# Kernel tuning notes

Hardware: AMD Instinct MI355X
Metric: run time of the kernel (lower is better)

Reference implementation:

```python
import jax, jax.numpy as jnp
import numpy as np

LN_EPS = 1e-5


def layernorm(x, gamma, beta):
    mu = x.mean(-1, keepdims=True)
    var = x.var(-1, keepdims=True)
    return (x - mu) / jnp.sqrt(var + LN_EPS) * gamma + beta


def setup_inputs() -> dict:
    key = jax.random.key(0)
    ks = jax.random.split(key, 8)
    B, S, H, F, V = 4, 512, 1024, 512, 32000
    def sc(k, shape, fan):
        return jax.random.normal(k, shape, jnp.float32) * (1.0 / np.sqrt(fan))
    return {
        "h": jax.random.normal(ks[0], (B, S, H), jnp.float32),
        "embedding_matrix": sc(ks[1], (V, F), F),
        "output_bias": jnp.zeros((V,), jnp.float32),
        "labels": jax.random.randint(ks[2], (B, S), 0, V),
        "W_hidden": sc(ks[3], (F, H), H),
        "b_hidden": jnp.zeros((F,), jnp.float32),
        "hidden_bias": jnp.zeros((F,), jnp.float32),
        "W_proj": sc(ks[4], (F, F), F),
        "projection_bias": jnp.zeros((F,), jnp.float32),
        "ln_gamma": jnp.ones((F,), jnp.float32),
        "ln_beta": jnp.zeros((F,), jnp.float32),
        "step_W": jnp.ones((F, F), jnp.float32),
        "step_b": jnp.ones((F,), jnp.float32),
    }


def _token_nll(logits, labels):
    # per-token cross entropy, reduction='none'
    logp = jax.nn.log_softmax(logits, axis=-1)
    return -jnp.take_along_axis(logp, labels[..., None], axis=-1)[..., 0]


def reference(h, embedding_matrix, output_bias, labels, W_hidden, b_hidden,
              hidden_bias, W_proj, projection_bias, ln_gamma, ln_beta,
              step_W, step_b):
    # ---- slow path + grads of summed slow loss wrt 4 params ----
    def slow_loss(Wh, hb, Wp, bp):
        v = jax.nn.relu(h @ Wh.T + b_hidden + hb)          # [B,S,F]
        o = layernorm(v @ Wp.T + bp, ln_gamma, ln_beta)    # [B,S,F]
        logits = o @ embedding_matrix.T + output_bias      # [B,S,V]
        return _token_nll(logits, labels).sum()

    gWh, ghb, gWp, gbp = jax.grad(slow_loss, argnums=(0, 1, 2, 3))(
        W_hidden, hidden_bias, W_proj, projection_bias)

    # ---- fast-weight path, vectorized over all timesteps ----
    # Per token: fast_w = W_proj - step_W * (v v^T) @ gWp
    #   (v v^T) @ gWp = outer(v, u) with u = v @ gWp, so
    #   v @ fast_w.T = v @ W_proj.T - v * ((v*u) @ step_W.T)   (no [F,F] per token)
    v = jax.nn.relu(h @ W_hidden.T + b_hidden + hidden_bias)  # [B,S,F]
    u = jnp.einsum('bsf,fg->bsg', v, gWp)                     # v^T gWp
    o_pre = v @ W_proj.T - v * jnp.einsum('bsf,gf->bsg', v * u, step_W)
    # fast_b = projection_bias - step_b * (v v^T) @ gbp = bp - step_b * v * (v.gbp)
    fast_b = projection_bias - step_b * v * (v @ gbp)[..., None]
    o_fast = layernorm(o_pre + fast_b, ln_gamma, ln_beta)     # [B,S,F]

    logits_fast = o_fast @ embedding_matrix.T + output_bias   # [B,S,V]
    fast_loss = _token_nll(logits_fast, labels)               # [B,S]
    return (fast_loss, gWh, ghb, gWp, gbp)
```

## Files before the change

kernel.cpp:

```cpp
#include <hip/hip_runtime.h>
#include <cstddef>
#include <math.h>

#define T_TOK 2048
#define F_DIM 512
#define H_DIM 1024
#define V_DIM 32000
#define VHALF 16000
#define NKC   5
#define KC    3200
#define LN_EPS 1e-5f
#define SHIFT 20.0f

typedef __attribute__((ext_vector_type(8))) short bf16x8;
typedef __attribute__((ext_vector_type(4))) float f32x4;

__device__ __forceinline__ unsigned short f2bf(float x) {
  unsigned int u = __float_as_uint(x);
  u += 0x7fffu + ((u >> 16) & 1u);
  return (unsigned short)(u >> 16);
}

__device__ __forceinline__ void gld16(const unsigned short* gsrc, unsigned short* ldst) {
  __builtin_amdgcn_global_load_lds(
      (const __attribute__((address_space(1))) unsigned int*)gsrc,
      (__attribute__((address_space(3))) unsigned int*)ldst, 16, 0, 0);
}

__device__ inline float wave_sum(float x) {
#pragma unroll
  for (int off = 32; off > 0; off >>= 1) x += __shfl_xor(x, off, 64);
  return x;
}

__global__ void zero_kernel(float* __restrict__ p, int n) {
  int i = blockIdx.x * 256 + threadIdx.x;
  if (i < n) p[i] = 0.f;
}

__global__ void zero4_kernel(float4* __restrict__ p, int n4) {
  int i = blockIdx.x * 256 + threadIdx.x;
  if (i < n4) {
    float4 z; z.x = 0.f; z.y = 0.f; z.z = 0.f; z.w = 0.f;
    p[i] = z;
  }
}

__global__ __launch_bounds__(256) void reduceK_kernel(
    const float4* __restrict__ parts, float4* __restrict__ out, int n4, int nslab) {
  const int i = blockIdx.x * 256 + threadIdx.x;
  if (i >= n4) return;
  float4 s = parts[i];
  for (int k = 1; k < nslab; ++k) {
    float4 p = parts[(size_t)k * n4 + i];
    s.x += p.x; s.y += p.y; s.z += p.z; s.w += p.w;
  }
  out[i] = s;
}

__global__ __launch_bounds__(256) void convT_kernel(
    const float* __restrict__ in, unsigned short* __restrict__ out, int R, int C) {
  __shared__ unsigned short tile[64][65];
  const int r0 = blockIdx.x * 64, c0 = blockIdx.y * 64;
  const int rr = threadIdx.x >> 4, cc4 = (threadIdx.x & 15) * 4;
#pragma unroll
  for (int ps = 0; ps < 4; ++ps) {
    const int row = ps * 16 + rr;
    float4 x = *(const float4*)&in[(size_t)(r0 + row) * C + c0 + cc4];
    tile[row][cc4 + 0] = f2bf(x.x); tile[row][cc4 + 1] = f2bf(x.y);
    tile[row][cc4 + 2] = f2bf(x.z); tile[row][cc4 + 3] = f2bf(x.w);
  }
  __syncthreads();
#pragma unroll
  for (int ps = 0; ps < 4; ++ps) {
    const int orow = ps * 16 + rr;
    ushort4 u;
    u.x = tile[cc4 + 0][orow]; u.y = tile[cc4 + 1][orow];
    u.z = tile[cc4 + 2][orow]; u.w = tile[cc4 + 3][orow];
    *(ushort4*)&out[(size_t)(c0 + orow) * R + r0 + cc4] = u;
  }
}

__global__ __launch_bounds__(256) void convertE_kernel(
    const float* __restrict__ E, unsigned short* __restrict__ Ebf,
    unsigned short* __restrict__ Etbf)
{
  __shared__ float tile[64][65];
  const int tid = threadIdx.x;
  const int v0 = blockIdx.x * 64, f0 = blockIdx.y * 64;
  const int r = tid >> 4, cq = (tid & 15) * 4;
#pragma unroll
  for (int ps = 0; ps < 4; ++ps) {
    const int row = ps * 16 + r;
    float4 x = *(const float4*)&E[(size_t)(v0 + row) * F_DIM + f0 + cq];
    tile[row][cq + 0] = x.x; tile[row][cq + 1] = x.y;
    tile[row][cq + 2] = x.z; tile[row][cq + 3] = x.w;
    ushort4 u; u.x = f2bf(x.x); u.y = f2bf(x.y); u.z = f2bf(x.z); u.w = f2bf(x.w);
    *(ushort4*)&Ebf[(size_t)(v0 + row) * F_DIM + f0 + cq] = u;
  }
  __syncthreads();
#pragma unroll
  for (int ps = 0; ps < 4; ++ps) {
    const int frow = ps * 16 + r;
    ushort4 u;
    u.x = f2bf(tile[cq + 0][frow]); u.y = f2bf(tile[cq + 1][frow]);
    u.z = f2bf(tile[cq + 2][frow]); u.w = f2bf(tile[cq + 3][frow]);
    *(ushort4*)&Etbf[(size_t)(f0 + frow) * V_DIM + v0 + cq] = u;
  }
}

__global__ __launch_bounds__(256, 2) void gemm_bf_nt_kernel(
    const unsigned short* __restrict__ A, const unsigned short* __restrict__ B,
    int M, int N, int K,
    const float* __restrict__ maskv,
    float* __restrict__ outf, int atomic_f)
{
  __shared__ __align__(16) unsigned short As[128 * 64];
  __shared__ __align__(16) unsigned short Bs[128 * 64];
  const int tid = threadIdx.x;
  const int w = tid >> 6, lane = tid & 63;
  const int c15 = lane & 15, q = lane >> 4;
  const int n0 = blockIdx.x * 128, m0 = blockIdx.y * 128;
  const int kc = K / gridDim.z;
  const int kbase = blockIdx.z * kc;
  const int mw = (w & 1) * 64, nw = (w >> 1) * 64;
  f32x4 acc[4][4];
#pragma unroll
  for (int mi = 0; mi < 4; ++mi)
#pragma unroll
    for (int nj = 0; nj < 4; ++nj) acc[mi][nj] = (f32x4){0.f, 0.f, 0.f, 0.f};
  for (int it = 0; it < kc / 64; ++it) {
    const int kb = kbase + it * 64;
#pragma unroll
    for (int i = 0; i < 4; ++i) {
      const int gid = (w * 4 + i) * 64 + lane;
      const int row = gid >> 3, col = gid & 7;
      const int colsrc = col ^ (row & 7);
      gld16(A + (size_t)(m0 + row) * K + kb + colsrc * 8, &As[(w * 4 + i) * 512]);
      gld16(B + (size_t)(n0 + row) * K + kb + colsrc * 8, &Bs[(w * 4 + i) * 512]);
    }
    __syncthreads();
#pragma unroll
    for (int kk = 0; kk < 2; ++kk) {
      const int g = (kk * 4 + q) ^ (c15 & 7);
      bf16x8 af[4], bfr[4];
#pragma unroll
      for (int mi = 0; mi < 4; ++mi) {
        const int row = mw + mi * 16 + c15;
        af[mi] = *(const bf16x8*)&As[(row * 8 + g) * 8];
      }
#pragma unroll
      for (int nj = 0; nj < 4; ++nj) {
        const int row = nw + nj * 16 + c15;
        bfr[nj] = *(const bf16x8*)&Bs[(row * 8 + g) * 8];
      }
#pragma unroll
      for (int mi = 0; mi < 4; ++mi)
#pragma unroll
        for (int nj = 0; nj < 4; ++nj)
          acc[mi][nj] = __builtin_amdgcn_mfma_f32_16x16x32_bf16(af[mi], bfr[nj], acc[mi][nj], 0, 0, 0);
    }
    __syncthreads();
  }
#pragma unroll
  for (int mi = 0; mi < 4; ++mi)
#pragma unroll
    for (int nj = 0; nj < 4; ++nj) {
      const int n = n0 + nw + nj * 16 + c15;
#pragma unroll
      for (int r = 0; r < 4; ++r) {
        const int m = m0 + mw + mi * 16 + q * 4 + r;
        const size_t idx = (size_t)m * N + n;
        float v = acc[mi][nj][r];
        if (maskv && !(maskv[idx] > 0.f)) v = 0.f;
        if (atomic_f) atomicAdd(outf + idx, v); else outf[idx] = v;
      }
    }
}

__global__ __launch_bounds__(256) void gemm_nt_kernel(
    const float* __restrict__ A, const float* __restrict__ A2,
    const float* __restrict__ B, float* __restrict__ C,
    int M, int N, int K,
    const float* __restrict__ bias1, const float* __restrict__ bias2, int relu)
{
  __shared__ float As[16][68];
  __shared__ float Bs[16][68];
  const int tid = threadIdx.x;
  const int m0 = blockIdx.y * 64, n0 = blockIdx.x * 64;
  const int ty = tid >> 4, tx = tid & 15;
  const int lrow = tid >> 2, lkq = (tid & 3) * 4;
  float acc[4][4] = {};
  for (int k0 = 0; k0 < K; k0 += 16) {
    float4 a4 = *(const float4*)(A + (size_t)(m0 + lrow) * K + k0 + lkq);
    if (A2) {
      float4 u4 = *(const float4*)(A2 + (size_t)(m0 + lrow) * K + k0 + lkq);
      a4.x *= u4.x; a4.y *= u4.y; a4.z *= u4.z; a4.w *= u4.w;
    }
    float4 b4 = *(const float4*)(B + (size_t)(n0 + lrow) * K + k0 + lkq);
    As[lkq+0][lrow] = a4.x; As[lkq+1][lrow] = a4.y; As[lkq+2][lrow] = a4.z; As[lkq+3][lrow] = a4.w;
    Bs[lkq+0][lrow] = b4.x; Bs[lkq+1][lrow] = b4.y; Bs[lkq+2][lrow] = b4.z; Bs[lkq+3][lrow] = b4.w;
    __syncthreads();
#pragma unroll
    for (int k = 0; k < 16; ++k) {
      float4 a = *(const float4*)&As[k][ty*4];
      float4 b = *(const float4*)&Bs[k][tx*4];
      float ar[4] = {a.x,a.y,a.z,a.w}, br[4] = {b.x,b.y,b.z,b.w};
#pragma unroll
      for (int i = 0; i < 4; ++i)
#pragma unroll
        for (int j = 0; j < 4; ++j) acc[i][j] = fmaf(ar[i], br[j], acc[i][j]);
    }
    __syncthreads();
  }
#pragma unroll
  for (int i = 0; i < 4; ++i) {
    const int m = m0 + ty*4 + i;
    float cr[4];
#pragma unroll
    for (int j = 0; j < 4; ++j) {
      const int n = n0 + tx*4 + j;
      float v = acc[i][j];
      if (bias1) v += bias1[n];
      if (bias2) v += bias2[n];
      if (relu) v = fmaxf(v, 0.f);
      cr[j] = v;
    }
    float4 c; c.x = cr[0]; c.y = cr[1]; c.z = cr[2]; c.w = cr[3];
    *(float4*)(C + (size_t)m * N + n0 + tx*4) = c;
  }
}

__global__ __launch_bounds__(256) void gemm_nn_kernel(
    const float* __restrict__ A, const float* __restrict__ B,
    float* __restrict__ C, int M, int N, int K)
{
  __shared__ float As[16][68];
  __shared__ float Bs[16][68];
  const int tid = threadIdx.x;
  const int m0 = blockIdx.y * 64, n0 = blockIdx.x * 64;
  const int ty = tid >> 4, tx = tid & 15;
  const int arow = tid >> 2, akq = (tid & 3) * 4;
  const int brow = tid >> 4, bcq = (tid & 15) * 4;
  float acc[4][4] = {};
  for (int k0 = 0; k0 < K; k0 += 16) {
    float4 a4 = *(const float4*)(A + (size_t)(m0 + arow) * K + k0 + akq);
    float4 b4 = *(const float4*)(B + (size_t)(k0 + brow) * N + n0 + bcq);
    As[akq+0][arow] = a4.x; As[akq+1][arow] = a4.y; As[akq+2][arow] = a4.z; As[akq+3][arow] = a4.w;
    *(float4*)&Bs[brow][bcq] = b4;
    __syncthreads();
#pragma unroll
    for (int k = 0; k < 16; ++k) {
      float4 a = *(const float4*)&As[k][ty*4];
      float4 b = *(const float4*)&Bs[k][tx*4];
      float ar[4] = {a.x,a.y,a.z,a.w}, br[4] = {b.x,b.y,b.z,b.w};
#pragma unroll
      for (int i = 0; i < 4; ++i)
#pragma unroll
        for (int j = 0; j < 4; ++j) acc[i][j] = fmaf(ar[i], br[j], acc[i][j]);
    }
    __syncthreads();
  }
#pragma unroll
  for (int i = 0; i < 4; ++i) {
    const int m = m0 + ty*4 + i;
    float4 c; c.x = acc[i][0]; c.y = acc[i][1]; c.z = acc[i][2]; c.w = acc[i][3];
    *(float4*)(C + (size_t)m * N + n0 + tx*4) = c;
  }
}

__global__ __launch_bounds__(256) void gemm_tn_kernel(
    const float* __restrict__ A, const float* __restrict__ B,
    float* __restrict__ C, int M, int N, int K)
{
  __shared__ float As[16][68];
  __shared__ float Bs[16][68];
  const int tid = threadIdx.x;
  const int m0 = blockIdx.y * 64, n0 = blockIdx.x * 64;
  const int ty = tid >> 4, tx = tid & 15;
  const int row = tid >> 4, cq = (tid & 15) * 4;
  const int kc = K / gridDim.z;
  const int kbase = blockIdx.z * kc;
  float* __restrict__ Co = C + (size_t)blockIdx.z * M * N;
  float acc[4][4] = {};
  for (int k0 = kbase; k0 < kbase + kc; k0 += 16) {
    float4 a4 = *(const float4*)(A + (size_t)(k0 + row) * M + m0 + cq);
    float4 b4 = *(const float4*)(B + (size_t)(k0 + row) * N + n0 + cq);
    *(float4*)&As[row][cq] = a4;
    *(float4*)&Bs[row][cq] = b4;
    __syncthreads();
#pragma unroll
    for (int k = 0; k < 16; ++k) {
      float4 a = *(const float4*)&As[k][ty*4];
      float4 b = *(const float4*)&Bs[k][tx*4];
      float ar[4] = {a.x,a.y,a.z,a.w}, br[4] = {b.x,b.y,b.z,b.w};
#pragma unroll
      for (int i = 0; i < 4; ++i)
#pragma unroll
        for (int j = 0; j < 4; ++j) acc[i][j] = fmaf(ar[i], br[j], acc[i][j]);
    }
    __syncthreads();
  }
#pragma unroll
  for (int i = 0; i < 4; ++i) {
    const int m = m0 + ty*4 + i;
    float4 c; c.x = acc[i][0]; c.y = acc[i][1]; c.z = acc[i][2]; c.w = acc[i][3];
    *(float4*)(Co + (size_t)m * N + n0 + tx*4) = c;
  }
}

__global__ __launch_bounds__(256) void ln_fwd_kernel(
    const float* __restrict__ p, const float* __restrict__ v,
    const float* __restrict__ tmat, const float* __restrict__ stepb,
    const float* __restrict__ sdot, const float* __restrict__ gamma,
    const float* __restrict__ beta, float* __restrict__ o,
    unsigned short* __restrict__ obf,
    float* __restrict__ mu_out, float* __restrict__ rstd_out, int fastmode)
{
  const int t = blockIdx.x * 4 + (threadIdx.x >> 6);
  const int lane = threadIdx.x & 63;
  const int f0 = lane * 4, f1 = 256 + lane * 4;
  const float* pr = p + (size_t)t * F_DIM;
  float4 x0 = *(const float4*)(pr + f0);
  float4 x1 = *(const float4*)(pr + f1);
  if (fastmode) {
    const float* vr = v + (size_t)t * F_DIM;
    const float* tr = tmat + (size_t)t * F_DIM;
    const float sdt = sdot[t];
    float4 v0 = *(const float4*)(vr + f0), v1 = *(const float4*)(vr + f1);
    float4 t0 = *(const float4*)(tr + f0), t1 = *(const float4*)(tr + f1);
    float4 s0 = *(const float4*)(stepb + f0), s1 = *(const float4*)(stepb + f1);
    x0.x -= v0.x * (t0.x + s0.x * sdt);
    x0.y -= v0.y * (t0.y + s0.y * sdt);
    x0.z -= v0.z * (t0.z + s0.z * sdt);
    x0.w -= v0.w * (t0.w + s0.w * sdt);
    x1.x -= v1.x * (t1.x + s1.x * sdt);
    x1.y -= v1.y * (t1.y + s1.y * sdt);
    x1.z -= v1.z * (t1.z + s1.z * sdt);
    x1.w -= v1.w * (t1.w + s1.w * sdt);
  }
  float s  = x0.x + x0.y + x0.z + x0.w + x1.x + x1.y + x1.z + x1.w;
  float ss = x0.x*x0.x + x0.y*x0.y + x0.z*x0.z + x0.w*x0.w
           + x1.x*x1.x + x1.y*x1.y + x1.z*x1.z + x1.w*x1.w;
  s = wave_sum(s); ss = wave_sum(ss);
  const float mu = s * (1.f / F_DIM);
  const float var = ss * (1.f / F_DIM) - mu * mu;
  const float rstd = rsqrtf(var + LN_EPS);
  float4 g0 = *(const float4*)(gamma + f0), g1 = *(const float4*)(gamma + f1);
  float4 b0 = *(const float4*)(beta + f0),  b1 = *(const float4*)(beta + f1);
  float4 y0, y1;
  y0.x = (x0.x - mu) * rstd * g0.x + b0.x;
  y0.y = (x0.y - mu) * rstd * g0.y + b0.y;
  y0.z = (x0.z - mu) * rstd * g0.z + b0.z;
  y0.w = (x0.w - mu) * rstd * g0.w + b0.w;
  y1.x = (x1.x - mu) * rstd * g1.x + b1.x;
  y1.y = (x1.y - mu) * rstd * g1.y + b1.y;
  y1.z = (x1.z - mu) * rstd * g1.z + b1.z;
  y1.w = (x1.w - mu) * rstd * g1.w + b1.w;
  if (o) {
    *(float4*)(o + (size_t)t * F_DIM + f0) = y0;
    *(float4*)(o + (size_t)t * F_DIM + f1) = y1;
  }
  ushort4 u0, u1;
  u0.x = f2bf(y0.x); u0.y = f2bf(y0.y); u0.z = f2bf(y0.z); u0.w = f2bf(y0.w);
  u1.x = f2bf(y1.x); u1.y = f2bf(y1.y); u1.z = f2bf(y1.z); u1.w = f2bf(y1.w);
  *(ushort4*)(obf + (size_t)t * F_DIM + f0) = u0;
  *(ushort4*)(obf + (size_t)t * F_DIM + f1) = u1;
  if (!fastmode && lane == 0) { mu_out[t] = mu; rstd_out[t] = rstd; }
}

__global__ __launch_bounds__(256) void ln_bwd_kernel(
    const float* __restrict__ U, const float* __restrict__ z_,
    const float* __restrict__ E,
    const int* __restrict__ labels, const float* __restrict__ gamma,
    const float* __restrict__ p, const float* __restrict__ mu_,
    const float* __restrict__ rstd_, float* __restrict__ dp,
    unsigned short* __restrict__ dpbf)
{
  const int t = blockIdx.x * 4 + (threadIdx.x >> 6);
  const int lane = threadIdx.x & 63;
  const int f0 = lane * 4, f1 = 256 + lane * 4;
  const int lab = labels[t];
  const float mu = mu_[t], rstd = rstd_[t];
  const float zr = 1.f / z_[t];
  const float* dor = U + (size_t)t * F_DIM;
  const float* er  = E + (size_t)lab * F_DIM;
  const float* pr  = p + (size_t)t * F_DIM;
  alignas(16) float d[8], e[8], g[8], x[8];
  *(float4*)&d[0] = *(const float4*)(dor + f0); *(float4*)&d[4] = *(const float4*)(dor + f1);
  *(float4*)&e[0] = *(const float4*)(er + f0);  *(float4*)&e[4] = *(const float4*)(er + f1);
  *(float4*)&g[0] = *(const float4*)(gamma + f0); *(float4*)&g[4] = *(const float4*)(gamma + f1);
  *(float4*)&x[0] = *(const float4*)(pr + f0);  *(float4*)&x[4] = *(const float4*)(pr + f1);
  float dh[8], xh[8];
  float s1 = 0.f, s2 = 0.f;
#pragma unroll
  for (int i = 0; i < 8; ++i) {
    dh[i] = (d[i] * zr - e[i]) * g[i];
    xh[i] = (x[i] - mu) * rstd;
    s1 += dh[i];
    s2 += dh[i] * xh[i];
  }
  s1 = wave_sum(s1); s2 = wave_sum(s2);
  const float c1 = s1 * (1.f / F_DIM), c2 = s2 * (1.f / F_DIM);
  alignas(16) float outv[8];
#pragma unroll
  for (int i = 0; i < 8; ++i) outv[i] = rstd * (dh[i] - c1 - xh[i] * c2);
  *(float4*)(dp + (size_t)t * F_DIM + f0) = *(float4*)&outv[0];
  *(float4*)(dp + (size_t)t * F_DIM + f1) = *(float4*)&outv[4];
  ushort4 u0, u1;
  u0.x = f2bf(outv[0]); u0.y = f2bf(outv[1]); u0.z = f2bf(outv[2]); u0.w = f2bf(outv[3]);
  u1.x = f2bf(outv[4]); u1.y = f2bf(outv[5]); u1.z = f2bf(outv[6]); u1.w = f2bf(outv[7]);
  *(ushort4*)(dpbf + (size_t)t * F_DIM + f0) = u0;
  *(ushort4*)(dpbf + (size_t)t * F_DIM + f1) = u1;
}

__global__ __launch_bounds__(256) void colsum_kernel(
    const float* __restrict__ X, float* __restrict__ out)
{
  const int f = blockIdx.x * 256 + threadIdx.x;
  const int t0 = blockIdx.y * 128;
  float s = 0.f;
  for (int r = 0; r < 128; ++r) s += X[(size_t)(t0 + r) * F_DIM + f];
  atomicAdd(out + f, s);
}

__global__ __launch_bounds__(256) void sdot_kernel(
    const float* __restrict__ v, const float* __restrict__ gbp,
    float* __restrict__ sd)
{
  const int t = blockIdx.x * 4 + (threadIdx.x >> 6);
  const int lane = threadIdx.x & 63;
  const int f0 = lane * 4, f1 = 256 + lane * 4;
  const float* vr = v + (size_t)t * F_DIM;
  float4 a0 = *(const float4*)(vr + f0), a1 = *(const float4*)(vr + f1);
  float4 b0 = *(const float4*)(gbp + f0), b1 = *(const float4*)(gbp + f1);
  float s = a0.x*b0.x + a0.y*b0.y + a0.z*b0.z + a0.w*b0.w
          + a1.x*b1.x + a1.y*b1.y + a1.z*b1.z + a1.w*b1.w;
  s = wave_sum(s);
  if (lane == 0) sd[t] = s;
}

__global__ __launch_bounds__(256, 2) void expsum_kernel(
    const unsigned short* __restrict__ obf, const unsigned short* __restrict__ Ebf,
    const float* __restrict__ ob, unsigned short* __restrict__ expS,
    float* __restrict__ z, int vbase)
{
  __shared__ __align__(16) unsigned short Es[128 * 64];
  __shared__ __align__(16) unsigned short Os[128 * 64];
  const int tid = threadIdx.x;
  const int w = tid >> 6, lane = tid & 63;
  const int c15 = lane & 15, q = lane >> 4;
  const int t0 = blockIdx.x * 128, v0 = vbase + blockIdx.y * 128;
  const int vw = v0 + (w & 1) * 64, tw = t0 + (w >> 1) * 64;
  f32x4 acc[4][4];
#pragma unroll
  for (int mi = 0; mi < 4; ++mi)
#pragma unroll
    for (int nj = 0; nj < 4; ++nj) acc[mi][nj] = (f32x4){0.f, 0.f, 0.f, 0.f};
  for (int it = 0; it < F_DIM / 64; ++it) {
    const int kb = it * 64;
#pragma unroll
    for (int i = 0; i < 4; ++i) {
      const int gid = (w * 4 + i) * 64 + lane;
      const int row = gid >> 3, col3 = gid & 7;
      const int colsrc = col3 ^ (row & 7);
      gld16(Ebf + (size_t)(v0 + row) * F_DIM + kb + colsrc * 8, &Es[(w * 4 + i) * 512]);
      gld16(obf + (size_t)(t0 + row) * F_DIM + kb + colsrc * 8, &Os[(w * 4 + i) * 512]);
    }
    __syncthreads();
#pragma unroll
    for (int kk = 0; kk < 2; ++kk) {
      const int g = (kk * 4 + q) ^ (c15 & 7);
      bf16x8 af[4], bfr[4];
#pragma unroll
      for (int mi = 0; mi < 4; ++mi) {
        const int row = (w & 1) * 64 + mi * 16 + c15;
        af[mi] = *(const bf16x8*)&Es[(row * 8 + g) * 8];
      }
#pragma unroll
      for (int nj = 0; nj < 4; ++nj) {
        const int row = (w >> 1) * 64 + nj * 16 + c15;
        bfr[nj] = *(const bf16x8*)&Os[(row * 8 + g) * 8];
      }
#pragma unroll
      for (int mi = 0; mi < 4; ++mi)
#pragma unroll
        for (int nj = 0; nj < 4; ++nj)
          acc[mi][nj] = __builtin_amdgcn_mfma_f32_16x16x32_bf16(af[mi], bfr[nj], acc[mi][nj], 0, 0, 0);
    }
    __syncthreads();
  }
  float obv[4][4];
#pragma unroll
  for (int mi = 0; mi < 4; ++mi)
    *(float4*)obv[mi] = *(const float4*)&ob[vw + mi * 16 + q * 4];
#pragma unroll
  for (int nj = 0; nj < 4; ++nj) {
    const int t = tw + nj * 16 + c15;
    float zsum = 0.f;
#pragma unroll
    for (int mi = 0; mi < 4; ++mi) {
      float e0 = __expf(acc[mi][nj][0] + obv[mi][0] - SHIFT);
      float e1 = __expf(acc[mi][nj][1] + obv[mi][1] - SHIFT);
      float e2 = __expf(acc[mi][nj][2] + obv[mi][2] - SHIFT);
      float e3 = __expf(acc[mi][nj][3] + obv[mi][3] - SHIFT);
      zsum += e0 + e1 + e2 + e3;
      if (expS) {
        const int vloc = vw - vbase + mi * 16 + q * 4;
        ushort4 u; u.x = f2bf(e0); u.y = f2bf(e1); u.z = f2bf(e2); u.w = f2bf(e3);
        *(ushort4*)&expS[(size_t)t * VHALF + vloc] = u;
      }
    }
    zsum += __shfl_xor(zsum, 16);
    zsum += __shfl_xor(zsum, 32);
    if (q == 0) atomicAdd(&z[t], zsum);
  }
}

__global__ __launch_bounds__(256, 2) void gemm_pe_kernel(
    const unsigned short* __restrict__ P, const unsigned short* __restrict__ Etbf,
    float* __restrict__ dO, int vbase)
{
  __shared__ __align__(16) unsigned short As[128 * 64];
  __shared__ __align__(16) unsigned short Bs[128 * 64];
  const int tid = threadIdx.x;
  const int w = tid >> 6, lane = tid & 63;
  const int c15 = lane & 15, q = lane >> 4;
  const int n0 = blockIdx.x * 128, m0 = blockIdx.y * 128;
  const int klbase = blockIdx.z * KC;
  const int mw = (w & 1) * 64, nw = (w >> 1) * 64;
  f32x4 acc[4][4];
#pragma unroll
  for (int mi = 0; mi < 4; ++mi)
#pragma unroll
    for (int nj = 0; nj < 4; ++nj) acc[mi][nj] = (f32x4){0.f, 0.f, 0.f, 0.f};
  for (int it = 0; it < KC / 64; ++it) {
    const int kl = klbase + it * 64;
#pragma unroll
    for (int i = 0; i < 4; ++i) {
      const int gid = (w * 4 + i) * 64 + lane;
      const int row = gid >> 3, col = gid & 7;
      const int colsrc = col ^ (row & 7);
      gld16(P + (size_t)(m0 + row) * VHALF + kl + colsrc * 8, &As[(w * 4 + i) * 512]);
      gld16(Etbf + (size_t)(n0 + row) * V_DIM + vbase + kl + colsrc * 8, &Bs[(w * 4 + i) * 512]);
    }
    __syncthreads();
#pragma unroll
    for (int kk = 0; kk < 2; ++kk) {
      const int g = (kk * 4 + q) ^ (c15 & 7);
      bf16x8 af[4], bfr[4];
#pragma unroll
      for (int mi = 0; mi < 4; ++mi) {
        const int row = mw + mi * 16 + c15;
        af[mi] = *(const bf16x8*)&As[(row * 8 + g) * 8];
      }
#pragma unroll
      for (int nj = 0; nj < 4; ++nj) {
        const int row = nw + nj * 16 + c15;
        bfr[nj] = *(const bf16x8*)&Bs[(row * 8 + g) * 8];
      }
#pragma unroll
      for (int mi = 0; mi < 4; ++mi)
#pragma unroll
        for (int nj = 0; nj < 4; ++nj)
          acc[mi][nj] = __builtin_amdgcn_mfma_f32_16x16x32_bf16(af[mi], bfr[nj], acc[mi][nj], 0, 0, 0);
    }
    __syncthreads();
  }
#pragma unroll
  for (int mi = 0; mi < 4; ++mi)
#pragma unroll
    for (int nj = 0; nj < 4; ++nj) {
      const int f = n0 + nw + nj * 16 + c15;
#pragma unroll
      for (int r = 0; r < 4; ++r) {
        const int t = m0 + mw + mi * 16 + q * 4 + r;
        atomicAdd(&dO[(size_t)t * F_DIM + f], acc[mi][nj][r]);
      }
    }
}

__global__ __launch_bounds__(256) void fast_loss_kernel(
    const float* __restrict__ of, const float* __restrict__ E,
    const float* __restrict__ ob, const int* __restrict__ labels,
    const float* __restrict__ zf,
    float* __restrict__ out)
{
  const int t = blockIdx.x * 4 + (threadIdx.x >> 6);
  const int lane = threadIdx.x & 63;
  const int f0 = lane * 4, f1 = 256 + lane * 4;
  const int lab = labels[t];
  const float* orow = of + (size_t)t * F_DIM;
  const float* er = E + (size_t)lab * F_DIM;
  float4 a0 = *(const float4*)(orow + f0), a1 = *(const float4*)(orow + f1);
  float4 b0 = *(const float4*)(er + f0),   b1 = *(const float4*)(er + f1);
  float s = a0.x*b0.x + a0.y*b0.y + a0.z*b0.z + a0.w*b0.w
          + a1.x*b1.x + a1.y*b1.y + a1.z*b1.z + a1.w*b1.w;
  s = wave_sum(s);
  if (lane == 0) out[t] = SHIFT + logf(zf[t]) - (s + ob[lab]);
}

extern "C" void kernel_launch(void* const* d_in, const int* in_sizes, int n_in,
                              void* d_out, int out_size, void* d_ws, size_t ws_size,
                              hipStream_t stream)
{
  const float* h      = (const float*)d_in[0];
  const float* E      = (const float*)d_in[1];
  const float* ob     = (const float*)d_in[2];
  const int*   labels = (const int*)d_in[3];
  const float* Wh     = (const float*)d_in[4];
  const float* bh     = (const float*)d_in[5];
  const float* hb     = (const float*)d_in[6];
  const float* Wp     = (const float*)d_in[7];
  const float* bp     = (const float*)d_in[8];
  const float* gamma  = (const float*)d_in[9];
  const float* beta   = (const float*)d_in[10];
  const float* stepW  = (const float*)d_in[11];
  const float* stepb  = (const float*)d_in[12];

  float* out_loss = (float*)d_out;
  float* out_gWh  = out_loss + T_TOK;
  float* out_ghb  = out_gWh + F_DIM * H_DIM;
  float* out_gWp  = out_ghb + F_DIM;
  float* out_gbp  = out_gWp + F_DIM * F_DIM;

  float* ws = (float*)d_ws;
  const size_t TF = (size_t)T_TOK * F_DIM;
  float* v_   = ws;
  float* p_   = ws + TF;
  float* dO_  = ws + 2 * TF;
  float* dp_  = ws + 3 * TF;
  float* dv_  = ws + 4 * TF;
  float* dv2_ = ws + 5 * TF;
  float* u_   = ws + 5 * TF;
  float* tm_  = ws + 6 * TF;
  float* of_  = ws + 7 * TF;
  float* sm   = ws + 8 * TF;
  float* mu_    = sm;
  float* rstd_  = sm + 2048;
  float* zs_    = sm + 4096;
  float* zf_    = sm + 6144;
  float* sd_    = sm + 8192;
  unsigned short* obf   = (unsigned short*)(sm + 10240);
  unsigned short* ofbf  = obf + TF;
  unsigned short* dpbf  = ofbf + TF;
  unsigned short* dvTbf = dpbf + TF;
  unsigned short* hbfT  = dvTbf + TF;
  unsigned short* WpTbf = hbfT + (size_t)T_TOK * H_DIM;
  unsigned short* Ebf   = WpTbf + (size_t)F_DIM * F_DIM;
  unsigned short* Etbf  = Ebf + (size_t)V_DIM * F_DIM;
  unsigned short* Pbuf  = Etbf + (size_t)V_DIM * F_DIM;

  (void)dv2_;

  zero4_kernel<<<(int)(TF / 4 / 256), 256, 0, stream>>>((float4*)dO_, (int)(TF / 4));
  zero_kernel<<<8, 256, 0, stream>>>(zs_, T_TOK);
  zero_kernel<<<8, 256, 0, stream>>>(zf_, T_TOK);
  zero_kernel<<<2, 256, 0, stream>>>(out_ghb, F_DIM);
  zero_kernel<<<2, 256, 0, stream>>>(out_gbp, F_DIM);
  zero4_kernel<<<F_DIM * H_DIM / 4 / 256, 256, 0, stream>>>((float4*)out_gWh, F_DIM * H_DIM / 4);

  convertE_kernel<<<dim3(V_DIM / 64, F_DIM / 64), 256, 0, stream>>>(E, Ebf, Etbf);
  convT_kernel<<<dim3(T_TOK / 64, H_DIM / 64), 256, 0, stream>>>(h, hbfT, T_TOK, H_DIM);
  convT_kernel<<<dim3(F_DIM / 64, F_DIM / 64), 256, 0, stream>>>(Wp, WpTbf, F_DIM, F_DIM);

  gemm_nt_kernel<<<dim3(F_DIM / 64, T_TOK / 64), 256, 0, stream>>>(
      h, nullptr, Wh, v_, T_TOK, F_DIM, H_DIM, bh, hb, 1);
  gemm_nt_kernel<<<dim3(8, 32), 256, 0, stream>>>(
      v_, nullptr, Wp, p_, T_TOK, F_DIM, F_DIM, bp, nullptr, 0);
  ln_fwd_kernel<<<512, 256, 0, stream>>>(
      p_, nullptr, nullptr, nullptr, nullptr, gamma, beta, nullptr, obf, mu_, rstd_, 0);
  expsum_kernel<<<dim3(T_TOK / 128, VHALF / 128), 256, 0, stream>>>(
      obf, Ebf, ob, Pbuf, zs_, 0);
  gemm_pe_kernel<<<dim3(F_DIM / 128, T_TOK / 128, NKC), 256, 0, stream>>>(Pbuf, Etbf, dO_, 0);
  expsum_kernel<<<dim3(T_TOK / 128, VHALF / 128), 256, 0, stream>>>(
      obf, Ebf, ob, Pbuf, zs_, VHALF);
  gemm_pe_kernel<<<dim3(F_DIM / 128, T_TOK / 128, NKC), 256, 0, stream>>>(Pbuf, Etbf, dO_, VHALF);
  ln_bwd_kernel<<<512, 256, 0, stream>>>(dO_, zs_, E, labels, gamma, p_, mu_, rstd_, dp_, dpbf);
  colsum_kernel<<<dim3(2, 16), 256, 0, stream>>>(dp_, out_gbp);
  gemm_tn_kernel<<<dim3(8, 8, 8), 256, 0, stream>>>(dp_, v_, dv_, F_DIM, F_DIM, T_TOK);
  reduceK_kernel<<<F_DIM * F_DIM / 4 / 256, 256, 0, stream>>>(
      (const float4*)dv_, (float4*)out_gWp, F_DIM * F_DIM / 4, 8);
  gemm_bf_nt_kernel<<<dim3(4, 16, 1), 256, 0, stream>>>(
      dpbf, WpTbf, T_TOK, F_DIM, F_DIM, v_, dv_, 0);
  colsum_kernel<<<dim3(2, 16), 256, 0, stream>>>(dv_, out_ghb);
  convT_kernel<<<dim3(T_TOK / 64, F_DIM / 64), 256, 0, stream>>>(dv_, dvTbf, T_TOK, F_DIM);
  gemm_bf_nt_kernel<<<dim3(8, 4, 4), 256, 0, stream>>>(
      dvTbf, hbfT, F_DIM, H_DIM, T_TOK, nullptr, out_gWh, 1);
  gemm_nn_kernel<<<dim3(8, 32), 256, 0, stream>>>(v_, out_gWp, u_, T_TOK, F_DIM, F_DIM);
  sdot_kernel<<<512, 256, 0, stream>>>(v_, out_gbp, sd_);
  gemm_nt_kernel<<<dim3(8, 32), 256, 0, stream>>>(
      v_, u_, stepW, tm_, T_TOK, F_DIM, F_DIM, nullptr, nullptr, 0);
  ln_fwd_kernel<<<512, 256, 0, stream>>>(
      p_, v_, tm_, stepb, sd_, gamma, beta, of_, ofbf, nullptr, nullptr, 1);
  expsum_kernel<<<dim3(T_TOK / 128, V_DIM / 128), 256, 0, stream>>>(
      ofbf, Ebf, ob, nullptr, zf_, 0);
  fast_loss_kernel<<<512, 256, 0, stream>>>(of_, E, ob, labels, zf_, out_loss);
}
```

Baseline: 703.2 us.

## Split-K the fp32 token GEMMs with a bias/ReLU reduce, and remap gemm_pe block order

The four fp32 SIMT GEMMs over the 2048-token dimension (h·Wh, v·Wp, v·gWp, (v*u)·stepW) now launch with a 4-way K split into dO_ scratch, and a reduce kernel sums the slabs and applies bias and ReLU. This quadruples the block count so the 256-block grids fill the GPU better, at the cost of extra scratch traffic and extra launches. The gemm_pe block index is remapped so blocks that share the same P rows and K chunk are scheduled near each other, aiming for better L2 reuse. The u/tm computations are also moved earlier, reusing the of_ buffer as scratch for u, and the dO_ zeroing is moved after its use as scratch.

```diff
diff --git a/kernel.cpp b/kernel.cpp
--- a/kernel.cpp
+++ b/kernel.cpp
@@ -47,13 +47,27 @@
 }
 
 __global__ __launch_bounds__(256) void reduceK_kernel(
-    const float4* __restrict__ parts, float4* __restrict__ out, int n4, int nslab) {
+    const float4* __restrict__ parts, float4* __restrict__ out, int n4, int nslab,
+    const float* __restrict__ bias1, const float* __restrict__ bias2, int relu) {
   const int i = blockIdx.x * 256 + threadIdx.x;
   if (i >= n4) return;
   float4 s = parts[i];
   for (int k = 1; k < nslab; ++k) {
     float4 p = parts[(size_t)k * n4 + i];
     s.x += p.x; s.y += p.y; s.z += p.z; s.w += p.w;
+  }
+  const int c = (i & (F_DIM / 4 - 1)) * 4;
+  if (bias1) {
+    float4 b = *(const float4*)(bias1 + c);
+    s.x += b.x; s.y += b.y; s.z += b.z; s.w += b.w;
+  }
+  if (bias2) {
+    float4 b = *(const float4*)(bias2 + c);
+    s.x += b.x; s.y += b.y; s.z += b.z; s.w += b.w;
+  }
+  if (relu) {
+    s.x = fmaxf(s.x, 0.f); s.y = fmaxf(s.y, 0.f);
+    s.z = fmaxf(s.z, 0.f); s.w = fmaxf(s.w, 0.f);
   }
   out[i] = s;
 }
@@ -190,8 +204,12 @@
   const int m0 = blockIdx.y * 64, n0 = blockIdx.x * 64;
   const int ty = tid >> 4, tx = tid & 15;
   const int lrow = tid >> 2, lkq = (tid & 3) * 4;
+  const int zc = gridDim.z;
+  const int kc = K / zc;
+  const int kbase = blockIdx.z * kc;
+  float* __restrict__ Co = C + (size_t)blockIdx.z * M * N;
   float acc[4][4] = {};
-  for (int k0 = 0; k0 < K; k0 += 16) {
+  for (int k0 = kbase; k0 < kbase + kc; k0 += 16) {
     float4 a4 = *(const float4*)(A + (size_t)(m0 + lrow) * K + k0 + lkq);
     if (A2) {
       float4 u4 = *(const float4*)(A2 + (size_t)(m0 + lrow) * K + k0 + lkq);
@@ -213,21 +231,30 @@
     }
     __syncthreads();
   }
-#pragma unroll
-  for (int i = 0; i < 4; ++i) {
-    const int m = m0 + ty*4 + i;
-    float cr[4];
-#pragma unroll
-    for (int j = 0; j < 4; ++j) {
-      const int n = n0 + tx*4 + j;
-      float v = acc[i][j];
-      if (bias1) v += bias1[n];
-      if (bias2) v += bias2[n];
-      if (relu) v = fmaxf(v, 0.f);
-      cr[j] = v;
-    }
-    float4 c; c.x = cr[0]; c.y = cr[1]; c.z = cr[2]; c.w = cr[3];
-    *(float4*)(C + (size_t)m * N + n0 + tx*4) = c;
+  if (zc == 1) {
+#pragma unroll
+    for (int i = 0; i < 4; ++i) {
+      const int m = m0 + ty*4 + i;
+      float cr[4];
+#pragma unroll
+      for (int j = 0; j < 4; ++j) {
+        const int n = n0 + tx*4 + j;
+        float v = acc[i][j];
+        if (bias1) v += bias1[n];
+        if (bias2) v += bias2[n];
+        if (relu) v = fmaxf(v, 0.f);
+        cr[j] = v;
+      }
+      float4 c; c.x = cr[0]; c.y = cr[1]; c.z = cr[2]; c.w = cr[3];
+      *(float4*)(C + (size_t)m * N + n0 + tx*4) = c;
+    }
+  } else {
+#pragma unroll
+    for (int i = 0; i < 4; ++i) {
+      const int m = m0 + ty*4 + i;
+      float4 c; c.x = acc[i][0]; c.y = acc[i][1]; c.z = acc[i][2]; c.w = acc[i][3];
+      *(float4*)(Co + (size_t)m * N + n0 + tx*4) = c;
+    }
   }
 }
 
@@ -242,8 +269,12 @@
   const int ty = tid >> 4, tx = tid & 15;
   const int arow = tid >> 2, akq = (tid & 3) * 4;
   const int brow = tid >> 4, bcq = (tid & 15) * 4;
+  const int zc = gridDim.z;
+  const int kc = K / zc;
+  const int kbase = blockIdx.z * kc;
+  float* __restrict__ Co = C + (size_t)blockIdx.z * M * N;
   float acc[4][4] = {};
-  for (int k0 = 0; k0 < K; k0 += 16) {
+  for (int k0 = kbase; k0 < kbase + kc; k0 += 16) {
     float4 a4 = *(const float4*)(A + (size_t)(m0 + arow) * K + k0 + akq);
     float4 b4 = *(const float4*)(B + (size_t)(k0 + brow) * N + n0 + bcq);
     As[akq+0][arow] = a4.x; As[akq+1][arow] = a4.y; As[akq+2][arow] = a4.z; As[akq+3][arow] = a4.w;
@@ -265,7 +296,7 @@
   for (int i = 0; i < 4; ++i) {
     const int m = m0 + ty*4 + i;
     float4 c; c.x = acc[i][0]; c.y = acc[i][1]; c.z = acc[i][2]; c.w = acc[i][3];
-    *(float4*)(C + (size_t)m * N + n0 + tx*4) = c;
+    *(float4*)(Co + (size_t)m * N + n0 + tx*4) = c;
   }
 }
 
@@ -526,8 +557,15 @@
   const int tid = threadIdx.x;
   const int w = tid >> 6, lane = tid & 63;
   const int c15 = lane & 15, q = lane >> 4;
-  const int n0 = blockIdx.x * 128, m0 = blockIdx.y * 128;
-  const int klbase = blockIdx.z * KC;
+  const int pf   = (int)blockIdx.x + 4 * (int)blockIdx.y + 64 * (int)blockIdx.z;
+  const int low  = pf & 7;
+  const int rest = pf >> 3;
+  const int j    = rest & 3;
+  const int ghi  = rest >> 2;
+  const int g    = ghi * 8 + low;
+  const int n0 = j * 128;
+  const int m0 = (g & 15) * 128;
+  const int klbase = (g >> 4) * KC;
   const int mw = (w & 1) * 64, nw = (w >> 1) * 64;
   f32x4 acc[4][4];
 #pragma unroll
@@ -547,17 +585,17 @@
     __syncthreads();
 #pragma unroll
     for (int kk = 0; kk < 2; ++kk) {
-      const int g = (kk * 4 + q) ^ (c15 & 7);
+      const int gg = (kk * 4 + q) ^ (c15 & 7);
       bf16x8 af[4], bfr[4];
 #pragma unroll
       for (int mi = 0; mi < 4; ++mi) {
         const int row = mw + mi * 16 + c15;
-        af[mi] = *(const bf16x8*)&As[(row * 8 + g) * 8];
+        af[mi] = *(const bf16x8*)&As[(row * 8 + gg) * 8];
       }
 #pragma unroll
       for (int nj = 0; nj < 4; ++nj) {
         const int row = nw + nj * 16 + c15;
-        bfr[nj] = *(const bf16x8*)&Bs[(row * 8 + g) * 8];
+        bfr[nj] = *(const bf16x8*)&Bs[(row * 8 + gg) * 8];
       }
 #pragma unroll
       for (int mi = 0; mi < 4; ++mi)
@@ -631,7 +669,6 @@
   float* dO_  = ws + 2 * TF;
   float* dp_  = ws + 3 * TF;
   float* dv_  = ws + 4 * TF;
-  float* dv2_ = ws + 5 * TF;
   float* u_   = ws + 5 * TF;
   float* tm_  = ws + 6 * TF;
   float* of_  = ws + 7 * TF;
@@ -651,9 +688,8 @@
   unsigned short* Etbf  = Ebf + (size_t)V_DIM * F_DIM;
   unsigned short* Pbuf  = Etbf + (size_t)V_DIM * F_DIM;
 
-  (void)dv2_;
-
-  zero4_kernel<<<(int)(TF / 4 / 256), 256, 0, stream>>>((float4*)dO_, (int)(TF / 4));
+  (void)u_;
+
   zero_kernel<<<8, 256, 0, stream>>>(zs_, T_TOK);
   zero_kernel<<<8, 256, 0, stream>>>(zf_, T_TOK);
   zero_kernel<<<2, 256, 0, stream>>>(out_ghb, F_DIM);
@@ -664,10 +700,15 @@
   convT_kernel<<<dim3(T_TOK / 64, H_DIM / 64), 256, 0, stream>>>(h, hbfT, T_TOK, H_DIM);
   convT_kernel<<<dim3(F_DIM / 64, F_DIM / 64), 256, 0, stream>>>(Wp, WpTbf, F_DIM, F_DIM);
 
-  gemm_nt_kernel<<<dim3(F_DIM / 64, T_TOK / 64), 256, 0, stream>>>(
-      h, nullptr, Wh, v_, T_TOK, F_DIM, H_DIM, bh, hb, 1);
-  gemm_nt_kernel<<<dim3(8, 32), 256, 0, stream>>>(
-      v_, nullptr, Wp, p_, T_TOK, F_DIM, F_DIM, bp, nullptr, 0);
+  gemm_nt_kernel<<<dim3(F_DIM / 64, T_TOK / 64, 4), 256, 0, stream>>>(
+      h, nullptr, Wh, dO_, T_TOK, F_DIM, H_DIM, nullptr, nullptr, 0);
+  reduceK_kernel<<<(int)(TF / 4 / 256), 256, 0, stream>>>(
+      (const float4*)dO_, (float4*)v_, (int)(TF / 4), 4, bh, hb, 1);
+  gemm_nt_kernel<<<dim3(8, 32, 4), 256, 0, stream>>>(
+      v_, nullptr, Wp, dO_, T_TOK, F_DIM, F_DIM, nullptr, nullptr, 0);
+  reduceK_kernel<<<(int)(TF / 4 / 256), 256, 0, stream>>>(
+      (const float4*)dO_, (float4*)p_, (int)(TF / 4), 4, bp, nullptr, 0);
+  zero4_kernel<<<(int)(TF / 4 / 256), 256, 0, stream>>>((float4*)dO_, (int)(TF / 4));
   ln_fwd_kernel<<<512, 256, 0, stream>>>(
       p_, nullptr, nullptr, nullptr, nullptr, gamma, beta, nullptr, obf, mu_, rstd_, 0);
   expsum_kernel<<<dim3(T_TOK / 128, VHALF / 128), 256, 0, stream>>>(
@@ -680,17 +721,21 @@
   colsum_kernel<<<dim3(2, 16), 256, 0, stream>>>(dp_, out_gbp);
   gemm_tn_kernel<<<dim3(8, 8, 8), 256, 0, stream>>>(dp_, v_, dv_, F_DIM, F_DIM, T_TOK);
   reduceK_kernel<<<F_DIM * F_DIM / 4 / 256, 256, 0, stream>>>(
-      (const float4*)dv_, (float4*)out_gWp, F_DIM * F_DIM / 4, 8);
+      (const float4*)dv_, (float4*)out_gWp, F_DIM * F_DIM / 4, 8, nullptr, nullptr, 0);
+  sdot_kernel<<<512, 256, 0, stream>>>(v_, out_gbp, sd_);
+  gemm_nn_kernel<<<dim3(8, 32, 4), 256, 0, stream>>>(v_, out_gWp, dO_, T_TOK, F_DIM, F_DIM);
+  reduceK_kernel<<<(int)(TF / 4 / 256), 256, 0, stream>>>(
+      (const float4*)dO_, (float4*)of_, (int)(TF / 4), 4, nullptr, nullptr, 0);
+  gemm_nt_kernel<<<dim3(8, 32, 4), 256, 0, stream>>>(
+      v_, of_, stepW, dO_, T_TOK, F_DIM, F_DIM, nullptr, nullptr, 0);
+  reduceK_kernel<<<(int)(TF / 4 / 256), 256, 0, stream>>>(
+      (const float4*)dO_, (float4*)tm_, (int)(TF / 4), 4, nullptr, nullptr, 0);
   gemm_bf_nt_kernel<<<dim3(4, 16, 1), 256, 0, stream>>>(
       dpbf, WpTbf, T_TOK, F_DIM, F_DIM, v_, dv_, 0);
   colsum_kernel<<<dim3(2, 16), 256, 0, stream>>>(dv_, out_ghb);
   convT_kernel<<<dim3(T_TOK / 64, F_DIM / 64), 256, 0, stream>>>(dv_, dvTbf, T_TOK, F_DIM);
   gemm_bf_nt_kernel<<<dim3(8, 4, 4), 256, 0, stream>>>(
       dvTbf, hbfT, F_DIM, H_DIM, T_TOK, nullptr, out_gWh, 1);
-  gemm_nn_kernel<<<dim3(8, 32), 256, 0, stream>>>(v_, out_gWp, u_, T_TOK, F_DIM, F_DIM);
-  sdot_kernel<<<512, 256, 0, stream>>>(v_, out_gbp, sd_);
-  gemm_nt_kernel<<<dim3(8, 32), 256, 0, stream>>>(
-      v_, u_, stepW, tm_, T_TOK, F_DIM, F_DIM, nullptr, nullptr, 0);
   ln_fwd_kernel<<<512, 256, 0, stream>>>(
       p_, v_, tm_, stepb, sd_, gamma, beta, of_, ofbf, nullptr, nullptr, 1);
   expsum_kernel<<<dim3(T_TOK / 128, V_DIM / 128), 256, 0, stream>>>(
```

Result: faster. 676.3 us (-3.8%).
